# Performance work log

Hardware: AMD Instinct MI355X
Metric: run time of the kernel (lower is better)

The kernel has to match this reference:

```python
import jax, jax.numpy as jnp
import numpy as np

B, T, D = 2, 128, 1024
H, R, Dk, Dv = 8, 8, 64, 64


def setup_inputs() -> dict:
    key = jax.random.key(0)
    ks = jax.random.split(key, 11)
    w = lambda k, shp: jax.random.normal(k, shp, dtype=jnp.float32) * 0.02
    return {
        "hidden_states": jax.random.normal(ks[0], (B, T, D), dtype=jnp.float32),
        "Wq": w(ks[1], (D, H * Dk)),
        "Wk": w(ks[2], (D, H * Dk)),
        "Wv": w(ks[3], (D, H * Dv)),
        "Wb": w(ks[4], (D, H * R)),
        "Wtg": w(ks[5], (D, H * R)),
        "mode_logits": jax.random.normal(ks[6], (H, R), dtype=jnp.float32) * 0.1,
        "log_decay": jax.random.normal(ks[7], (H, R), dtype=jnp.float32) * 0.1,
        "omega_log_scale": jax.random.normal(ks[8], (H, R), dtype=jnp.float32) * 0.1,
        "Wg": w(ks[9], (D, H * Dv)),
        "Wo": w(ks[10], (H * Dv, D)),
    }


def _forward(x, Wq, Wk, Wv, Wb, Wtg, mode_logits, log_decay, omega_log_scale, Wg, Wo):
    b, t, _ = x.shape
    # projections
    q = (x @ Wq).reshape(b, t, H, Dk)
    k = (x @ Wk).reshape(b, t, H, Dk)
    v = (x @ Wv).reshape(b, t, H, Dv)
    beta = jax.nn.sigmoid((x @ Wb).reshape(b, t, H, R))
    tg = jax.nn.sigmoid((x @ Wtg).reshape(b, t, H, R))
    # spectral mode parameters
    pair_idx = jnp.arange(0, Dk, 2, dtype=jnp.float32)
    inv_freq = 1.0 / (10000.0 ** (pair_idx / Dk))            # [Dk/2]
    omega = jnp.exp(omega_log_scale)[..., None] * inv_freq    # [H,R,Dk/2]
    omega_full = jnp.repeat(omega, 2, axis=-1)                # [H,R,Dk] (repeat_interleave)
    cos_w = jnp.cos(omega_full)[None, :, :, None, :]          # [1,H,R,1,Dk]
    sin_w = jnp.sin(omega_full)[None, :, :, None, :]
    rho = jnp.exp(-jax.nn.softplus(log_decay))                # [H,R]
    mode_w = jax.nn.softmax(mode_logits, axis=-1)             # [H,R]

    # time-major for scan
    qT = jnp.moveaxis(q, 1, 0)
    kT = jnp.moveaxis(k, 1, 0)
    vT = jnp.moveaxis(v, 1, 0)
    betaT = jnp.moveaxis(beta, 1, 0)
    tgT = jnp.moveaxis(tg, 1, 0)

    def step(carry, xs):
        sr, si = carry                      # [B,H,R,Dv,Dk] each
        q_t, k_t, v_t, b_t, g_t = xs
        decay = (g_t * rho)[..., None, None]            # [B,H,R,1,1]
        rot_r = decay * (cos_w * sr - sin_w * si)
        rot_i = decay * (sin_w * sr + cos_w * si)
        pred = jnp.einsum('bhrvk,bhk->bhrv', rot_r, k_t)
        err = v_t[:, :, None, :] - pred                  # [B,H,R,Dv]
        write = err[..., None] * k_t[:, :, None, None, :]
        sr_new = rot_r + b_t[..., None, None] * write
        read = jnp.einsum('bhrvk,bhk->bhrv', sr_new, q_t)
        y = jnp.einsum('bhrv,hr->bhv', read, mode_w)     # [B,H,Dv]
        return (sr_new, rot_i), y

    s0 = jnp.zeros((b, H, R, Dv, Dk), dtype=x.dtype)
    _, ys = jax.lax.scan(step, (s0, s0), (qT, kT, vT, betaT, tgT))
    o = jnp.moveaxis(ys, 0, 1)                           # [B,T,H,Dv]
    gate = jax.nn.sigmoid((x @ Wg).reshape(b, t, H, Dv))
    o = (o * gate).reshape(b, t, H * Dv)
    return o @ Wo


def reference(hidden_states, Wq, Wk, Wv, Wb, Wtg, mode_logits, log_decay,
              omega_log_scale, Wg, Wo):
    return _forward(hidden_states, Wq, Wk, Wv, Wb, Wtg, mode_logits,
                    log_decay, omega_log_scale, Wg, Wo)
```

## Files before the change

### kernel.cpp

```cpp
#include <hip/hip_runtime.h>
#include <math.h>

#define T_ 128
#define NPROJ 2176
#define CH 32

typedef __attribute__((ext_vector_type(8))) short short8;
typedef __attribute__((ext_vector_type(4))) float float4v;
typedef __attribute__((ext_vector_type(2))) float float2v;

__device__ __forceinline__ ushort f2bf(float x) {
    unsigned u = __float_as_uint(x);
    u += 0x7FFF + ((u >> 16) & 1);
    return (ushort)(u >> 16);
}
__device__ __forceinline__ unsigned pack_bf(float a, float b) {
    unsigned ua = (__float_as_uint(a) + 0x8000u) >> 16;
    unsigned ub = (__float_as_uint(b) + 0x8000u) & 0xffff0000u;
    return ua | ub;
}
__device__ __forceinline__ float bf_lo(unsigned w) { return __uint_as_float(w << 16); }
__device__ __forceinline__ float bf_hi(unsigned w) { return __uint_as_float(w & 0xffff0000u); }

template<int CTRL>
__device__ __forceinline__ float dpp_add(float x) {
    int xi = __float_as_int(x);
    int yi = __builtin_amdgcn_update_dpp(xi, xi, CTRL, 0xF, 0xF, false);
    return x + __int_as_float(yi);
}

__global__ __launch_bounds__(256) void prep_kernel(
    const float* __restrict__ x,
    const float* __restrict__ Wq, const float* __restrict__ Wk,
    const float* __restrict__ Wv, const float* __restrict__ Wb,
    const float* __restrict__ Wtg, const float* __restrict__ Wg,
    const float* __restrict__ Wo,
    const float* __restrict__ mode_logits, const float* __restrict__ log_decay,
    const float* __restrict__ ols,
    float* __restrict__ cosw, float* __restrict__ sinw,
    float* __restrict__ rho, float* __restrict__ modew,
    ushort* __restrict__ xb, ushort* __restrict__ wtb, ushort* __restrict__ wotb,
    float* __restrict__ Acomb)
{
    __shared__ ushort tile[64][68];
    const int blk = blockIdx.x, tid = threadIdx.x;
    if (blk < 16) {
        int idx = blk * 256 + tid;
        if (idx >= 64 * 64) return;
        int t = idx >> 6;
        int k = idx & 63;
        int h = t >> 3;
        if (k == 0) {
            float ld = log_decay[t];
            rho[t] = 1.0f / (1.0f + expf(ld));
            float m = -1e30f;
            for (int i = 0; i < 8; i++) m = fmaxf(m, mode_logits[h * 8 + i]);
            float sum = 0.0f;
            for (int i = 0; i < 8; i++) sum += expf(mode_logits[h * 8 + i] - m);
            modew[t] = expf(mode_logits[t] - m) / sum;
        }
        float osc = expf(ols[t]);
        int p = k >> 1;
        float invf = expf(-((float)(2 * p) / 64.0f) * logf(10000.0f));
        float w = osc * invf;
        cosw[idx] = cosf(w);
        sinw[idx] = sinf(w);
        return;
    }
    if (blk < 80) {
        int base = (blk - 16) * 4096 + tid * 16;
        float4 f0 = *(const float4*)&x[base];
        float4 f1 = *(const float4*)&x[base + 4];
        float4 f2 = *(const float4*)&x[base + 8];
        float4 f3 = *(const float4*)&x[base + 12];
        short8 o0, o1;
        o0[0]=f2bf(f0.x); o0[1]=f2bf(f0.y); o0[2]=f2bf(f0.z); o0[3]=f2bf(f0.w);
        o0[4]=f2bf(f1.x); o0[5]=f2bf(f1.y); o0[6]=f2bf(f1.z); o0[7]=f2bf(f1.w);
        o1[0]=f2bf(f2.x); o1[1]=f2bf(f2.y); o1[2]=f2bf(f2.z); o1[3]=f2bf(f2.w);
        o1[4]=f2bf(f3.x); o1[5]=f2bf(f3.y); o1[6]=f2bf(f3.z); o1[7]=f2bf(f3.w);
        *(short8*)&xb[base] = o0;
        *(short8*)&xb[base + 8] = o1;
        return;
    }
    if (blk >= 752) {
        int base = (blk - 752) * 4096 + tid * 16;
        float4 z = make_float4(0.f, 0.f, 0.f, 0.f);
        *(float4*)&Acomb[base] = z;
        *(float4*)&Acomb[base + 4] = z;
        *(float4*)&Acomb[base + 8] = z;
        *(float4*)&Acomb[base + 12] = z;
        return;
    }
    const float* src; int ld, c0, n0, k0, ldd; ushort* dst;
    if (blk < 624) {
        int b3 = blk - 80; int nt = b3 >> 4, kt = b3 & 15;
        n0 = nt * 64; k0 = kt * 64;
        if (n0 < 512)       { src = Wq;  c0 = n0;        ld = 512; }
        else if (n0 < 1024) { src = Wk;  c0 = n0 - 512;  ld = 512; }
        else if (n0 < 1536) { src = Wv;  c0 = n0 - 1024; ld = 512; }
        else if (n0 < 1600) { src = Wb;  c0 = n0 - 1536; ld = 64;  }
        else if (n0 < 1664) { src = Wtg; c0 = n0 - 1600; ld = 64;  }
        else                { src = Wg;  c0 = n0 - 1664; ld = 512; }
        dst = wtb; ldd = 1024;
    } else {
        int b4 = blk - 624; int nt = b4 >> 3, kt = b4 & 7;
        n0 = nt * 64; k0 = kt * 64;
        src = Wo; c0 = n0; ld = 1024; dst = wotb; ldd = 512;
    }
    #pragma unroll
    for (int rep = 0; rep < 4; rep++) {
        int k = rep * 16 + (tid >> 4);
        int nc = (tid & 15) * 4;
        float4 f = *(const float4*)&src[(size_t)(k0 + k) * ld + c0 + nc];
        tile[nc + 0][k] = f2bf(f.x);
        tile[nc + 1][k] = f2bf(f.y);
        tile[nc + 2][k] = f2bf(f.z);
        tile[nc + 3][k] = f2bf(f.w);
    }
    __syncthreads();
    #pragma unroll
    for (int rep = 0; rep < 4; rep++) {
        int n = rep * 16 + (tid >> 4);
        int kc = (tid & 15) * 4;
        uint2 uu = *(const uint2*)&tile[n][kc];
        *(uint2*)&dst[(size_t)(n0 + n) * ldd + k0 + kc] = uu;
    }
}

__global__ __launch_bounds__(256, 2) void proj_mfma(const ushort* __restrict__ Ab,
        const ushort* __restrict__ BTb, float* __restrict__ proj)
{
    __shared__ ushort sA[2][64][40];
    __shared__ ushort sB[2][64][40];
    const int n0 = blockIdx.x * 64, m0 = blockIdx.y * 64;
    const int tid = threadIdx.x;
    const int lane = tid & 63, w = tid >> 6;
    const int wm = w & 1, wn = w >> 1;
    const int l16 = lane & 15, quad = lane >> 4;
    const int srow = tid >> 2, skq = (tid & 3) * 8;
    const ushort* Ag = Ab + (size_t)(m0 + srow) * 1024 + skq;
    const ushort* Bg = BTb + (size_t)(n0 + srow) * 1024 + skq;
    short8 ra = *(const short8*)Ag;
    short8 rb = *(const short8*)Bg;
    float4v acc00 = {0,0,0,0}, acc01 = {0,0,0,0}, acc10 = {0,0,0,0}, acc11 = {0,0,0,0};
    for (int kt = 0; kt < 32; kt++) {
        const int cb = kt & 1;
        *(short8*)&sA[cb][srow][skq] = ra;
        *(short8*)&sB[cb][srow][skq] = rb;
        __syncthreads();
        if (kt + 1 < 32) {
            ra = *(const short8*)(Ag + (kt + 1) * 32);
            rb = *(const short8*)(Bg + (kt + 1) * 32);
        }
        short8 a0 = *(const short8*)&sA[cb][wm * 32 + l16][quad * 8];
        short8 a1 = *(const short8*)&sA[cb][wm * 32 + 16 + l16][quad * 8];
        short8 b0 = *(const short8*)&sB[cb][wn * 32 + l16][quad * 8];
        short8 b1 = *(const short8*)&sB[cb][wn * 32 + 16 + l16][quad * 8];
        acc00 = __builtin_amdgcn_mfma_f32_16x16x32_bf16(a0, b0, acc00, 0, 0, 0);
        acc01 = __builtin_amdgcn_mfma_f32_16x16x32_bf16(a0, b1, acc01, 0, 0, 0);
        acc10 = __builtin_amdgcn_mfma_f32_16x16x32_bf16(a1, b0, acc10, 0, 0, 0);
        acc11 = __builtin_amdgcn_mfma_f32_16x16x32_bf16(a1, b1, acc11, 0, 0, 0);
    }
    const bool sig = (n0 >= 1536);
    const int colb = n0 + wn * 32 + l16;
    const int rowb = m0 + wm * 32 + quad * 4;
    #pragma unroll
    for (int r2 = 0; r2 < 4; r2++) {
        float v00 = acc00[r2], v01 = acc01[r2], v10 = acc10[r2], v11 = acc11[r2];
        if (sig) {
            v00 = 1.0f / (1.0f + expf(-v00));
            v01 = 1.0f / (1.0f + expf(-v01));
            v10 = 1.0f / (1.0f + expf(-v10));
            v11 = 1.0f / (1.0f + expf(-v11));
        }
        proj[(size_t)(rowb + r2) * NPROJ + colb] = v00;
        proj[(size_t)(rowb + r2) * NPROJ + colb + 16] = v01;
        proj[(size_t)(rowb + 16 + r2) * NPROJ + colb] = v10;
        proj[(size_t)(rowb + 16 + r2) * NPROJ + colb + 16] = v11;
    }
}

__global__ __launch_bounds__(256, 2) void scan_kernel(const float* __restrict__ proj,
        const float* __restrict__ cosw, const float* __restrict__ sinw,
        const float* __restrict__ rho, const float* __restrict__ modew,
        float* __restrict__ Acomb)
{
    __shared__ uint2 qks[2][CH][16][2];
    __shared__ float2 vg[2][CH][16];
    __shared__ float sc4[2][CH][4];
    __shared__ float obuf[CH][16];

    const int bi = blockIdx.x;
    const int s  = bi & 3;
    const int hr = (bi >> 2) & 63;
    const int b  = bi >> 8;
    const int h = hr >> 3, r = hr & 7;
    const int tid = threadIdx.x;
    const int vl = tid >> 4;
    const int kl = tid & 15;

    float2v cw0, cw1, sw0, sw1;
    cw0.x = cosw[hr * 64 + kl * 4 + 0]; cw0.y = cosw[hr * 64 + kl * 4 + 1];
    cw1.x = cosw[hr * 64 + kl * 4 + 2]; cw1.y = cosw[hr * 64 + kl * 4 + 3];
    sw0.x = sinw[hr * 64 + kl * 4 + 0]; sw0.y = sinw[hr * 64 + kl * 4 + 1];
    sw1.x = sinw[hr * 64 + kl * 4 + 2]; sw1.y = sinw[hr * 64 + kl * 4 + 3];
    const float rho_hr = rho[hr];
    const float mw = modew[hr];
    float2v sr0 = {0,0}, sr1 = {0,0}, si0 = {0,0}, si1 = {0,0};

    const float* pb = proj + (size_t)b * T_ * NPROJ;
    const int qbase = h * 64;
    const int kbase = 512 + h * 64;
    const int vbase = 1024 + h * 64 + s * 16;
    const int gbase = 1664 + h * 64 + s * 16;
    const int boff  = 1536 + h * 8 + r;
    const int goff  = 1600 + h * 8 + r;

    {
        #pragma unroll
        for (int rep = 0; rep < 4; rep++) {
            int idx = rep * 256 + tid;
            int t = idx >> 5, sub = idx & 31;
            const float* row = pb + (size_t)t * NPROJ;
            float4 f = *(const float4*)(row + (sub < 16 ? qbase + sub * 4
                                                        : kbase + (sub - 16) * 4));
            uint2 pk2; pk2.x = pack_bf(f.x, f.y); pk2.y = pack_bf(f.z, f.w);
            qks[0][t][sub & 15][sub < 16 ? 1 : 0] = pk2;
        }
        #pragma unroll
        for (int rep = 0; rep < 2; rep++) {
            int idx = rep * 256 + tid;
            int t = idx >> 4, v2 = idx & 15;
            const float* row = pb + (size_t)t * NPROJ;
            vg[0][t][v2] = make_float2(row[vbase + v2], row[gbase + v2]);
        }
        if (tid < CH)            sc4[0][tid][0]      = pb[(size_t)tid * NPROJ + boff];
        else if (tid < 2 * CH)   sc4[0][tid - CH][1] = pb[(size_t)(tid - CH) * NPROJ + goff];
    }
    __syncthreads();

    float* dstb = Acomb + ((size_t)b * 128) * 512 + h * 64 + s * 16;

    for (int c = 0; c < T_ / CH; c++) {
        const int cb = c & 1, nb = cb ^ 1;
        const bool have = (c + 1 < T_ / CH);

        float4 g_qk[4]; float2 g_vg[2]; float g_sc = 0.0f;
        if (have) {
            const int t0 = (c + 1) * CH;
            #pragma unroll
            for (int rep = 0; rep < 4; rep++) {
                int idx = rep * 256 + tid;
                int t = idx >> 5, sub = idx & 31;
                const float* row = pb + (size_t)(t0 + t) * NPROJ;
                g_qk[rep] = *(const float4*)(row + (sub < 16 ? qbase + sub * 4
                                                             : kbase + (sub - 16) * 4));
            }
            #pragma unroll
            for (int rep = 0; rep < 2; rep++) {
                int idx = rep * 256 + tid;
                int t = idx >> 4, v2 = idx & 15;
                const float* row = pb + (size_t)(t0 + t) * NPROJ;
                g_vg[rep] = make_float2(row[vbase + v2], row[gbase + v2]);
            }
            if (tid < CH)          g_sc = pb[(size_t)(t0 + tid) * NPROJ + boff];
            else if (tid < 2 * CH) g_sc = pb[(size_t)(t0 + tid - CH) * NPROJ + goff];
        }

        {
            int t = tid >> 3, j = tid & 7;
            uint4 wa = *(const uint4*)&qks[cb][t][2 * j][0];
            uint4 wb = *(const uint4*)&qks[cb][t][2 * j + 1][0];
            float p = bf_lo(wa.x) * bf_lo(wa.z) + bf_hi(wa.x) * bf_hi(wa.z)
                    + bf_lo(wa.y) * bf_lo(wa.w) + bf_hi(wa.y) * bf_hi(wa.w)
                    + bf_lo(wb.x) * bf_lo(wb.z) + bf_hi(wb.x) * bf_hi(wb.z)
                    + bf_lo(wb.y) * bf_lo(wb.w) + bf_hi(wb.y) * bf_hi(wb.w);
            p = dpp_add<0xB1>(p);
            p = dpp_add<0x4E>(p);
            p = dpp_add<0x141>(p);
            if (j == 0) sc4[cb][t][2] = p;
        }
        if (c > 0) {
            #pragma unroll
            for (int rep = 0; rep < 2; rep++) {
                int idx = rep * 256 + tid;
                int t = idx >> 4, v2 = idx & 15;
                atomicAdd(dstb + (size_t)((c - 1) * CH + t) * 512 + v2, obuf[t][v2]);
            }
        }
        __syncthreads();

        const float2* vgb = &vg[cb][0][0];
        const float4* svb = (const float4*)&sc4[cb][0][0];

        uint4 w = *(const uint4*)&qks[cb][0][kl][0];
        float4 sv = svb[0];
        float2 vgv = vgb[vl];
        #pragma unroll
        for (int t = 0; t < CH; t++) {
            uint4 w_n; float4 sv_n; float2 vg_n;
            if (t + 1 < CH) {
                w_n = *(const uint4*)&qks[cb][t + 1][kl][0];
                sv_n = svb[t + 1];
                vg_n = vgb[(t + 1) * 16 + vl];
            }

            float2v k0; k0.x = bf_lo(w.x); k0.y = bf_hi(w.x);
            float2v k1; k1.x = bf_lo(w.y); k1.y = bf_hi(w.y);
            float2v q0; q0.x = bf_lo(w.z); q0.y = bf_hi(w.z);
            float2v q1; q1.x = bf_lo(w.w); q1.y = bf_hi(w.w);

            const float decay = sv.y * rho_hr;
            float2v t1 = cw0 * sr0 - sw0 * si0;
            float2v u1 = sw0 * sr0 + cw0 * si0;
            float2v t2 = cw1 * sr1 - sw1 * si1;
            float2v u2 = sw1 * sr1 + cw1 * si1;
            float2v d2; d2.x = decay; d2.y = decay;
            float2v rr0 = d2 * t1, rr1 = d2 * t2;
            si0 = d2 * u1; si1 = d2 * u2;

            float2v pk2 = rr0 * k0 + rr1 * k1;
            float2v pq2 = rr0 * q0 + rr1 * q1;
            float pk = pk2.x + pk2.y;
            float pq = pq2.x + pq2.y;
            pk = dpp_add<0xB1>(pk);  pq = dpp_add<0xB1>(pq);
            pk = dpp_add<0x4E>(pk);  pq = dpp_add<0x4E>(pq);
            pk = dpp_add<0x141>(pk); pq = dpp_add<0x141>(pq);
            pk = dpp_add<0x140>(pk); pq = dpp_add<0x140>(pq);

            const float sc = sv.x * (vgv.x - pk);
            float2v sc2; sc2.x = sc; sc2.y = sc;
            sr0 = rr0 + sc2 * k0;
            sr1 = rr1 + sc2 * k1;
            const float rp = pq + sc * sv.z;
            if (kl == 0) obuf[t][vl] = mw * rp * vgv.y;

            w = w_n; sv = sv_n; vgv = vg_n;
        }

        if (have) {
            #pragma unroll
            for (int rep = 0; rep < 4; rep++) {
                int idx = rep * 256 + tid;
                int t = idx >> 5, sub = idx & 31;
                float4 f = g_qk[rep];
                uint2 pk2; pk2.x = pack_bf(f.x, f.y); pk2.y = pack_bf(f.z, f.w);
                qks[nb][t][sub & 15][sub < 16 ? 1 : 0] = pk2;
            }
            #pragma unroll
            for (int rep = 0; rep < 2; rep++) {
                int idx = rep * 256 + tid;
                int t = idx >> 4, v2 = idx & 15;
                vg[nb][t][v2] = g_vg[rep];
            }
            if (tid < CH)          sc4[nb][tid][0]      = g_sc;
            else if (tid < 2 * CH) sc4[nb][tid - CH][1] = g_sc;
        }
        __syncthreads();
    }
    #pragma unroll
    for (int rep = 0; rep < 2; rep++) {
        int idx = rep * 256 + tid;
        int t = idx >> 4, v2 = idx & 15;
        atomicAdd(dstb + (size_t)(3 * CH + t) * 512 + v2, obuf[t][v2]);
    }
}

__global__ __launch_bounds__(256, 2) void out_mfma(const float* __restrict__ Af,
        const ushort* __restrict__ BTb, float* __restrict__ C)
{
    __shared__ ushort sA[2][64][40];
    __shared__ ushort sB[2][64][40];
    const int n0 = blockIdx.x * 64, m0 = blockIdx.y * 64;
    const int tid = threadIdx.x;
    const int lane = tid & 63, w = tid >> 6;
    const int wm = w & 1, wn = w >> 1;
    const int l16 = lane & 15, quad = lane >> 4;
    const int srow = tid >> 2, skq = (tid & 3) * 8;
    const float* Ag = Af + (size_t)(m0 + srow) * 512 + skq;
    const ushort* Bg = BTb + (size_t)(n0 + srow) * 512 + skq;
    float4 fa0 = *(const float4*)Ag;
    float4 fa1 = *(const float4*)(Ag + 4);
    short8 rb = *(const short8*)Bg;
    float4v acc00 = {0,0,0,0}, acc01 = {0,0,0,0}, acc10 = {0,0,0,0}, acc11 = {0,0,0,0};
    for (int kt = 0; kt < 16; kt++) {
        const int cb = kt & 1;
        short8 ra;
        ra[0]=f2bf(fa0.x); ra[1]=f2bf(fa0.y); ra[2]=f2bf(fa0.z); ra[3]=f2bf(fa0.w);
        ra[4]=f2bf(fa1.x); ra[5]=f2bf(fa1.y); ra[6]=f2bf(fa1.z); ra[7]=f2bf(fa1.w);
        *(short8*)&sA[cb][srow][skq] = ra;
        *(short8*)&sB[cb][srow][skq] = rb;
        __syncthreads();
        if (kt + 1 < 16) {
            fa0 = *(const float4*)(Ag + (kt + 1) * 32);
            fa1 = *(const float4*)(Ag + (kt + 1) * 32 + 4);
            rb = *(const short8*)(Bg + (kt + 1) * 32);
        }
        short8 a0 = *(const short8*)&sA[cb][wm * 32 + l16][quad * 8];
        short8 a1 = *(const short8*)&sA[cb][wm * 32 + 16 + l16][quad * 8];
        short8 b0 = *(const short8*)&sB[cb][wn * 32 + l16][quad * 8];
        short8 b1 = *(const short8*)&sB[cb][wn * 32 + 16 + l16][quad * 8];
        acc00 = __builtin_amdgcn_mfma_f32_16x16x32_bf16(a0, b0, acc00, 0, 0, 0);
        acc01 = __builtin_amdgcn_mfma_f32_16x16x32_bf16(a0, b1, acc01, 0, 0, 0);
        acc10 = __builtin_amdgcn_mfma_f32_16x16x32_bf16(a1, b0, acc10, 0, 0, 0);
        acc11 = __builtin_amdgcn_mfma_f32_16x16x32_bf16(a1, b1, acc11, 0, 0, 0);
    }
    const int colb = n0 + wn * 32 + l16;
    const int rowb = m0 + wm * 32 + quad * 4;
    #pragma unroll
    for (int r2 = 0; r2 < 4; r2++) {
        C[(size_t)(rowb + r2) * 1024 + colb] = acc00[r2];
        C[(size_t)(rowb + r2) * 1024 + colb + 16] = acc01[r2];
        C[(size_t)(rowb + 16 + r2) * 1024 + colb] = acc10[r2];
        C[(size_t)(rowb + 16 + r2) * 1024 + colb + 16] = acc11[r2];
    }
}

extern "C" void kernel_launch(void* const* d_in, const int* in_sizes, int n_in,
                              void* d_out, int out_size, void* d_ws, size_t ws_size,
                              hipStream_t stream) {
    const float* x   = (const float*)d_in[0];
    const float* Wq  = (const float*)d_in[1];
    const float* Wk  = (const float*)d_in[2];
    const float* Wv  = (const float*)d_in[3];
    const float* Wb  = (const float*)d_in[4];
    const float* Wtg = (const float*)d_in[5];
    const float* ml  = (const float*)d_in[6];
    const float* ldc = (const float*)d_in[7];
    const float* ols = (const float*)d_in[8];
    const float* Wg  = (const float*)d_in[9];
    const float* Wo  = (const float*)d_in[10];
    float* out = (float*)d_out;

    float* ws = (float*)d_ws;
    float* proj    = ws;
    float* cosw    = proj + 256 * NPROJ;
    float* sinw    = cosw + 4096;
    float* rho     = sinw + 4096;
    float* modew   = rho + 64;
    ushort* xb     = (ushort*)(modew + 64);
    ushort* wotb   = (ushort*)((float*)xb + 131072);
    float*  Acomb  = (float*)wotb + 262144;
    ushort* wtb    = (ushort*)(Acomb + 131072);

    prep_kernel<<<784, 256, 0, stream>>>(x, Wq, Wk, Wv, Wb, Wtg, Wg, Wo,
                                         ml, ldc, ols, cosw, sinw, rho, modew,
                                         xb, wtb, wotb, Acomb);
    proj_mfma<<<dim3(34, 4), 256, 0, stream>>>(xb, wtb, proj);
    scan_kernel<<<512, 256, 0, stream>>>(proj, cosw, sinw, rho, modew, Acomb);
    out_mfma<<<dim3(16, 4), 256, 0, stream>>>(Acomb, wotb, out);
}
```

Before: 136.9 us.

## Deepen global prefetch in GEMMs, keep q/k fp32 in scan, fold rho into gate

The projection and output GEMMs now prefetch two K-tiles ahead into register double buffers instead of one. This is meant to hide more global load latency. The scan kernel stores q/k in LDS as fp32 instead of packed bf16, which removes the pack/unpack ALU work and doubles the LDS footprint. It also prefetches per-timestep operands two steps ahead. The decay rate rho is multiplied into the temporal gate sigmoid in the projection epilogue, so the scan no longer does that multiply.

Result: slower. 241.0 us (+75.9%).

```diff
diff --git a/kernel.cpp b/kernel.cpp
--- a/kernel.cpp
+++ b/kernel.cpp
@@ -14,13 +14,6 @@
     u += 0x7FFF + ((u >> 16) & 1);
     return (ushort)(u >> 16);
 }
-__device__ __forceinline__ unsigned pack_bf(float a, float b) {
-    unsigned ua = (__float_as_uint(a) + 0x8000u) >> 16;
-    unsigned ub = (__float_as_uint(b) + 0x8000u) & 0xffff0000u;
-    return ua | ub;
-}
-__device__ __forceinline__ float bf_lo(unsigned w) { return __uint_as_float(w << 16); }
-__device__ __forceinline__ float bf_hi(unsigned w) { return __uint_as_float(w & 0xffff0000u); }
 
 template<int CTRL>
 __device__ __forceinline__ float dpp_add(float x) {
@@ -128,7 +121,8 @@
 }
 
 __global__ __launch_bounds__(256, 2) void proj_mfma(const ushort* __restrict__ Ab,
-        const ushort* __restrict__ BTb, float* __restrict__ proj)
+        const ushort* __restrict__ BTb, const float* __restrict__ rho,
+        float* __restrict__ proj)
 {
     __shared__ ushort sA[2][64][40];
     __shared__ ushort sB[2][64][40];
@@ -140,17 +134,20 @@
     const int srow = tid >> 2, skq = (tid & 3) * 8;
     const ushort* Ag = Ab + (size_t)(m0 + srow) * 1024 + skq;
     const ushort* Bg = BTb + (size_t)(n0 + srow) * 1024 + skq;
-    short8 ra = *(const short8*)Ag;
-    short8 rb = *(const short8*)Bg;
+    short8 ra2[2], rb2[2];
+    ra2[0] = *(const short8*)Ag;
+    rb2[0] = *(const short8*)Bg;
+    ra2[1] = *(const short8*)(Ag + 32);
+    rb2[1] = *(const short8*)(Bg + 32);
     float4v acc00 = {0,0,0,0}, acc01 = {0,0,0,0}, acc10 = {0,0,0,0}, acc11 = {0,0,0,0};
     for (int kt = 0; kt < 32; kt++) {
         const int cb = kt & 1;
-        *(short8*)&sA[cb][srow][skq] = ra;
-        *(short8*)&sB[cb][srow][skq] = rb;
+        *(short8*)&sA[cb][srow][skq] = ra2[cb];
+        *(short8*)&sB[cb][srow][skq] = rb2[cb];
         __syncthreads();
-        if (kt + 1 < 32) {
-            ra = *(const short8*)(Ag + (kt + 1) * 32);
-            rb = *(const short8*)(Bg + (kt + 1) * 32);
+        if (kt + 2 < 32) {
+            ra2[cb] = *(const short8*)(Ag + (kt + 2) * 32);
+            rb2[cb] = *(const short8*)(Bg + (kt + 2) * 32);
         }
         short8 a0 = *(const short8*)&sA[cb][wm * 32 + l16][quad * 8];
         short8 a1 = *(const short8*)&sA[cb][wm * 32 + 16 + l16][quad * 8];
@@ -162,16 +159,21 @@
         acc11 = __builtin_amdgcn_mfma_f32_16x16x32_bf16(a1, b1, acc11, 0, 0, 0);
     }
     const bool sig = (n0 >= 1536);
+    float m0c = 1.0f, m1c = 1.0f;
+    if (n0 == 1600) {
+        m0c = rho[wn * 32 + l16];
+        m1c = rho[wn * 32 + l16 + 16];
+    }
     const int colb = n0 + wn * 32 + l16;
     const int rowb = m0 + wm * 32 + quad * 4;
     #pragma unroll
     for (int r2 = 0; r2 < 4; r2++) {
         float v00 = acc00[r2], v01 = acc01[r2], v10 = acc10[r2], v11 = acc11[r2];
         if (sig) {
-            v00 = 1.0f / (1.0f + expf(-v00));
-            v01 = 1.0f / (1.0f + expf(-v01));
-            v10 = 1.0f / (1.0f + expf(-v10));
-            v11 = 1.0f / (1.0f + expf(-v11));
+            v00 = m0c / (1.0f + expf(-v00));
+            v01 = m1c / (1.0f + expf(-v01));
+            v10 = m0c / (1.0f + expf(-v10));
+            v11 = m1c / (1.0f + expf(-v11));
         }
         proj[(size_t)(rowb + r2) * NPROJ + colb] = v00;
         proj[(size_t)(rowb + r2) * NPROJ + colb + 16] = v01;
@@ -182,10 +184,9 @@
 
 __global__ __launch_bounds__(256, 2) void scan_kernel(const float* __restrict__ proj,
         const float* __restrict__ cosw, const float* __restrict__ sinw,
-        const float* __restrict__ rho, const float* __restrict__ modew,
-        float* __restrict__ Acomb)
+        const float* __restrict__ modew, float* __restrict__ Acomb)
 {
-    __shared__ uint2 qks[2][CH][16][2];
+    __shared__ float4 qks[2][CH][16][3];
     __shared__ float2 vg[2][CH][16];
     __shared__ float sc4[2][CH][4];
     __shared__ float obuf[CH][16];
@@ -194,7 +195,8 @@
     const int s  = bi & 3;
     const int hr = (bi >> 2) & 63;
     const int b  = bi >> 8;
-    const int h = hr >> 3, r = hr & 7;
+    const int h = hr >> 3;
+    const int r = hr & 7;
     const int tid = threadIdx.x;
     const int vl = tid >> 4;
     const int kl = tid & 15;
@@ -204,7 +206,6 @@
     cw1.x = cosw[hr * 64 + kl * 4 + 2]; cw1.y = cosw[hr * 64 + kl * 4 + 3];
     sw0.x = sinw[hr * 64 + kl * 4 + 0]; sw0.y = sinw[hr * 64 + kl * 4 + 1];
     sw1.x = sinw[hr * 64 + kl * 4 + 2]; sw1.y = sinw[hr * 64 + kl * 4 + 3];
-    const float rho_hr = rho[hr];
     const float mw = modew[hr];
     float2v sr0 = {0,0}, sr1 = {0,0}, si0 = {0,0}, si1 = {0,0};
 
@@ -224,8 +225,7 @@
             const float* row = pb + (size_t)t * NPROJ;
             float4 f = *(const float4*)(row + (sub < 16 ? qbase + sub * 4
                                                         : kbase + (sub - 16) * 4));
-            uint2 pk2; pk2.x = pack_bf(f.x, f.y); pk2.y = pack_bf(f.z, f.w);
-            qks[0][t][sub & 15][sub < 16 ? 1 : 0] = pk2;
+            qks[0][t][sub & 15][sub < 16 ? 1 : 0] = f;
         }
         #pragma unroll
         for (int rep = 0; rep < 2; rep++) {
@@ -269,12 +269,12 @@
 
         {
             int t = tid >> 3, j = tid & 7;
-            uint4 wa = *(const uint4*)&qks[cb][t][2 * j][0];
-            uint4 wb = *(const uint4*)&qks[cb][t][2 * j + 1][0];
-            float p = bf_lo(wa.x) * bf_lo(wa.z) + bf_hi(wa.x) * bf_hi(wa.z)
-                    + bf_lo(wa.y) * bf_lo(wa.w) + bf_hi(wa.y) * bf_hi(wa.w)
-                    + bf_lo(wb.x) * bf_lo(wb.z) + bf_hi(wb.x) * bf_hi(wb.z)
-                    + bf_lo(wb.y) * bf_lo(wb.w) + bf_hi(wb.y) * bf_hi(wb.w);
+            float4 ka = qks[cb][t][2 * j][0];
+            float4 qa = qks[cb][t][2 * j][1];
+            float4 kb = qks[cb][t][2 * j + 1][0];
+            float4 qb = qks[cb][t][2 * j + 1][1];
+            float p = ka.x * qa.x + ka.y * qa.y + ka.z * qa.z + ka.w * qa.w
+                    + kb.x * qb.x + kb.y * qb.y + kb.z * qb.z + kb.w * qb.w;
             p = dpp_add<0xB1>(p);
             p = dpp_add<0x4E>(p);
             p = dpp_add<0x141>(p);
@@ -293,24 +293,30 @@
         const float2* vgb = &vg[cb][0][0];
         const float4* svb = (const float4*)&sc4[cb][0][0];
 
-        uint4 w = *(const uint4*)&qks[cb][0][kl][0];
-        float4 sv = svb[0];
-        float2 vgv = vgb[vl];
+        float4 kvp[2], qvp[2], svp[2]; float2 vgp[2];
+        kvp[0] = qks[cb][0][kl][0]; qvp[0] = qks[cb][0][kl][1];
+        svp[0] = svb[0];            vgp[0] = vgb[vl];
+        kvp[1] = qks[cb][1][kl][0]; qvp[1] = qks[cb][1][kl][1];
+        svp[1] = svb[1];            vgp[1] = vgb[16 + vl];
+
         #pragma unroll
         for (int t = 0; t < CH; t++) {
-            uint4 w_n; float4 sv_n; float2 vg_n;
-            if (t + 1 < CH) {
-                w_n = *(const uint4*)&qks[cb][t + 1][kl][0];
-                sv_n = svb[t + 1];
-                vg_n = vgb[(t + 1) * 16 + vl];
-            }
-
-            float2v k0; k0.x = bf_lo(w.x); k0.y = bf_hi(w.x);
-            float2v k1; k1.x = bf_lo(w.y); k1.y = bf_hi(w.y);
-            float2v q0; q0.x = bf_lo(w.z); q0.y = bf_hi(w.z);
-            float2v q1; q1.x = bf_lo(w.w); q1.y = bf_hi(w.w);
-
-            const float decay = sv.y * rho_hr;
+            const int cur = t & 1;
+            float4 kv = kvp[cur], qv = qvp[cur], sv = svp[cur];
+            float2 vgv = vgp[cur];
+            if (t + 2 < CH) {
+                kvp[cur] = qks[cb][t + 2][kl][0];
+                qvp[cur] = qks[cb][t + 2][kl][1];
+                svp[cur] = svb[t + 2];
+                vgp[cur] = vgb[(t + 2) * 16 + vl];
+            }
+
+            float2v k0; k0.x = kv.x; k0.y = kv.y;
+            float2v k1; k1.x = kv.z; k1.y = kv.w;
+            float2v q0; q0.x = qv.x; q0.y = qv.y;
+            float2v q1; q1.x = qv.z; q1.y = qv.w;
+
+            const float decay = sv.y;
             float2v t1 = cw0 * sr0 - sw0 * si0;
             float2v u1 = sw0 * sr0 + cw0 * si0;
             float2v t2 = cw1 * sr1 - sw1 * si1;
@@ -334,8 +340,6 @@
             sr1 = rr1 + sc2 * k1;
             const float rp = pq + sc * sv.z;
             if (kl == 0) obuf[t][vl] = mw * rp * vgv.y;
-
-            w = w_n; sv = sv_n; vgv = vg_n;
         }
 
         if (have) {
@@ -343,9 +347,7 @@
             for (int rep = 0; rep < 4; rep++) {
                 int idx = rep * 256 + tid;
                 int t = idx >> 5, sub = idx & 31;
-                float4 f = g_qk[rep];
-                uint2 pk2; pk2.x = pack_bf(f.x, f.y); pk2.y = pack_bf(f.z, f.w);
-                qks[nb][t][sub & 15][sub < 16 ? 1 : 0] = pk2;
+                qks[nb][t][sub & 15][sub < 16 ? 1 : 0] = g_qk[rep];
             }
             #pragma unroll
             for (int rep = 0; rep < 2; rep++) {
@@ -379,22 +381,26 @@
     const int srow = tid >> 2, skq = (tid & 3) * 8;
     const float* Ag = Af + (size_t)(m0 + srow) * 512 + skq;
     const ushort* Bg = BTb + (size_t)(n0 + srow) * 512 + skq;
-    float4 fa0 = *(const float4*)Ag;
-    float4 fa1 = *(const float4*)(Ag + 4);
-    short8 rb = *(const short8*)Bg;
+    float4 fa0[2], fa1[2]; short8 rb2[2];
+    fa0[0] = *(const float4*)Ag;
+    fa1[0] = *(const float4*)(Ag + 4);
+    rb2[0] = *(const short8*)Bg;
+    fa0[1] = *(const float4*)(Ag + 32);
+    fa1[1] = *(const float4*)(Ag + 36);
+    rb2[1] = *(const short8*)(Bg + 32);
     float4v acc00 = {0,0,0,0}, acc01 = {0,0,0,0}, acc10 = {0,0,0,0}, acc11 = {0,0,0,0};
     for (int kt = 0; kt < 16; kt++) {
         const int cb = kt & 1;
         short8 ra;
-        ra[0]=f2bf(fa0.x); ra[1]=f2bf(fa0.y); ra[2]=f2bf(fa0.z); ra[3]=f2bf(fa0.w);
-        ra[4]=f2bf(fa1.x); ra[5]=f2bf(fa1.y); ra[6]=f2bf(fa1.z); ra[7]=f2bf(fa1.w);
+        ra[0]=f2bf(fa0[cb].x); ra[1]=f2bf(fa0[cb].y); ra[2]=f2bf(fa0[cb].z); ra[3]=f2bf(fa0[cb].w);
+        ra[4]=f2bf(fa1[cb].x); ra[5]=f2bf(fa1[cb].y); ra[6]=f2bf(fa1[cb].z); ra[7]=f2bf(fa1[cb].w);
         *(short8*)&sA[cb][srow][skq] = ra;
-        *(short8*)&sB[cb][srow][skq] = rb;
+        *(short8*)&sB[cb][srow][skq] = rb2[cb];
         __syncthreads();
-        if (kt + 1 < 16) {
-            fa0 = *(const float4*)(Ag + (kt + 1) * 32);
-            fa1 = *(const float4*)(Ag + (kt + 1) * 32 + 4);
-            rb = *(const short8*)(Bg + (kt + 1) * 32);
+        if (kt + 2 < 16) {
+            fa0[cb] = *(const float4*)(Ag + (kt + 2) * 32);
+            fa1[cb] = *(const float4*)(Ag + (kt + 2) * 32 + 4);
+            rb2[cb] = *(const short8*)(Bg + (kt + 2) * 32);
         }
         short8 a0 = *(const short8*)&sA[cb][wm * 32 + l16][quad * 8];
         short8 a1 = *(const short8*)&sA[cb][wm * 32 + 16 + l16][quad * 8];
@@ -446,7 +452,7 @@
     prep_kernel<<<784, 256, 0, stream>>>(x, Wq, Wk, Wv, Wb, Wtg, Wg, Wo,
                                          ml, ldc, ols, cosw, sinw, rho, modew,
                                          xb, wtb, wotb, Acomb);
-    proj_mfma<<<dim3(34, 4), 256, 0, stream>>>(xb, wtb, proj);
-    scan_kernel<<<512, 256, 0, stream>>>(proj, cosw, sinw, rho, modew, Acomb);
+    proj_mfma<<<dim3(34, 4), 256, 0, stream>>>(xb, wtb, rho, proj);
+    scan_kernel<<<512, 256, 0, stream>>>(proj, cosw, sinw, modew, Acomb);
     out_mfma<<<dim3(16, 4), 256, 0, stream>>>(Acomb, wotb, out);
 }
```
